# Optimization experiments

Measured on AMD Instinct MI355X. Metric: run time of the kernel, lower is better.

The kernel has to match this reference:

```python
import jax, jax.numpy as jnp
import numpy as np

B, S, D = 4, 2048, 2048          # batch, seq_len, num_hiddens (= query/key/value size)
H = 16                           # num_heads
DH = D // H                      # head dim = shared K/V projection dim


def setup_inputs() -> dict:
    key = jax.random.key(0)
    ks = jax.random.split(key, 11)
    s_in = 1.0 / np.sqrt(D)
    return {
        "q": jax.random.normal(ks[0], (B, S, D), jnp.float32),
        "k": jax.random.normal(ks[1], (B, S, D), jnp.float32),
        "v": jax.random.normal(ks[2], (B, S, D), jnp.float32),
        "Wq": jax.random.normal(ks[3], (D, D), jnp.float32) * s_in,
        "bq": jnp.zeros((D,), jnp.float32),
        "Wk": jax.random.normal(ks[4], (D, DH), jnp.float32) * s_in,
        "bk": jnp.zeros((DH,), jnp.float32),
        "Wv": jax.random.normal(ks[5], (D, DH), jnp.float32) * s_in,
        "bv": jnp.zeros((DH,), jnp.float32),
        "Wo": jax.random.normal(ks[6], (D, D), jnp.float32) * s_in,
        "bo": jnp.zeros((D,), jnp.float32),
    }


def reference(q, k, v, Wq, bq, Wk, bk, Wv, bv, Wo, bo):
    # Projections
    qh = (q @ Wq + bq).reshape(B, S, H, DH).transpose(0, 2, 1, 3)  # [B,H,S,DH]
    kh = k @ Wk + bk                                               # [B,S,DH] shared K head
    vh = v @ Wv + bv                                               # [B,S,DH] shared V head
    # Scaled dot-product attention with broadcast-shared K/V (no copies)
    scores = jnp.einsum('bhqd,bkd->bhqk', qh, kh) / jnp.sqrt(jnp.float32(DH))
    attn = jax.nn.softmax(scores, axis=-1)                          # [B,H,S,S]
    out = jnp.einsum('bhqk,bkd->bhqd', attn, vh)                    # [B,H,S,DH]
    out = out.transpose(0, 2, 1, 3).reshape(B, S, D)                # merge heads
    return out @ Wo + bo
```

## Files before the change

### kernel.cpp

```cpp
#include <hip/hip_runtime.h>
#include <stdint.h>

#define B_  4
#define S_  2048
#define D_  2048
#define H_  16
#define DH_ 128
#define M_  (B_*S_)

typedef unsigned short u16;
typedef __bf16 bf16x8 __attribute__((ext_vector_type(8)));
typedef float  f32x4  __attribute__((ext_vector_type(4)));
typedef u16    u16x4  __attribute__((ext_vector_type(4)));

__device__ __forceinline__ u16 f2bf(float f){
  unsigned x = __float_as_uint(f);
  x += 0x7fffu + ((x >> 16) & 1u);
  return (u16)(x >> 16);
}

__device__ __forceinline__ unsigned pkbf(float lo, float hi){
  unsigned r;
  asm("v_cvt_pk_bf16_f32 %0, %1, %2" : "=v"(r) : "v"(lo), "v"(hi));
  return r;
}

__device__ __forceinline__ void stage16(const void* g, void* lds_base){
  __builtin_amdgcn_global_load_lds(
      (const __attribute__((address_space(1))) void*)g,
      (__attribute__((address_space(3))) void*)lds_base, 16, 0, 0);
}

__device__ __forceinline__ f32x4 mfma16(bf16x8 a, bf16x8 b, f32x4 c){
  return __builtin_amdgcn_mfma_f32_16x16x32_bf16(a, b, c, 0, 0, 0);
}

__global__ void cvt_bf16(const float* __restrict__ s, u16* __restrict__ d, int n4){
  int i = blockIdx.x * 256 + threadIdx.x;
  if (i >= n4) return;
  float4 f = ((const float4*)s)[i];
  u16x4 u = { f2bf(f.x), f2bf(f.y), f2bf(f.z), f2bf(f.w) };
  ((u16x4*)d)[i] = u;
}

__global__ void cvt_bf16_2(const float* __restrict__ s0, const float* __restrict__ s1,
                           u16* __restrict__ d0, u16* __restrict__ d1, int n4){
  const float* s = blockIdx.y ? s1 : s0;
  u16*        d = blockIdx.y ? d1 : d0;
  int i = blockIdx.x * 256 + threadIdx.x;
  if (i >= n4) return;
  float4 f = ((const float4*)s)[i];
  u16x4 u = { f2bf(f.x), f2bf(f.y), f2bf(f.z), f2bf(f.w) };
  ((u16x4*)d)[i] = u;
}

__global__ void transpose_bf(const float* __restrict__ W, u16* __restrict__ WT, int K, int N){
  __shared__ float tl[32][33];
  int n0 = blockIdx.x * 32, k0 = blockIdx.y * 32;
  int tx = threadIdx.x, ty = threadIdx.y;
  for (int r = 0; r < 4; r++)
    tl[ty + 8*r][tx] = W[(size_t)(k0 + ty + 8*r) * N + n0 + tx];
  __syncthreads();
  for (int r = 0; r < 4; r++)
    WT[(size_t)(n0 + ty + 8*r) * K + k0 + tx] = f2bf(tl[tx][ty + 8*r]);
}

__global__ void transpose_vh(const u16* __restrict__ vh, u16* __restrict__ vhT){
  __shared__ u16 tl[32][33];
  int b = blockIdx.z, d0 = blockIdx.x * 32, s0 = blockIdx.y * 32;
  int tx = threadIdx.x, ty = threadIdx.y;
  for (int r = 0; r < 4; r++)
    tl[ty + 8*r][tx] = vh[(size_t)(b * S_ + s0 + ty + 8*r) * DH_ + d0 + tx];
  __syncthreads();
  for (int r = 0; r < 4; r++)
    vhT[(size_t)(b * DH_ + d0 + ty + 8*r) * S_ + s0 + tx] = tl[tx][ty + 8*r];
}

template<int OUTF32>
__global__ __launch_bounds__(512, 1) void gemm256(const u16* __restrict__ A,
    const u16* __restrict__ BT, const float* __restrict__ bias, void* __restrict__ Cv)
{
  __shared__ alignas(16) u16 AB[2][2][2 * 128 * 64];
  const int t = threadIdx.x, lane = t & 63, wave = t >> 6;
  const int quad = lane >> 4, lcol = lane & 15;
  const int wr = wave >> 1, wc = wave & 1;
  const int bid = blockIdx.x;
  const int swz = (bid & 7) * 32 + (bid >> 3);
  const int n0 = (swz & 7) * 256, m0 = (swz >> 3) * 256;
  const int NT = 2048 / 64;

  auto stageH = [&](const u16* g, int grow0, int kcol0, u16* lb){
    #pragma unroll
    for (int i = 0; i < 2; i++){
      int l = (i*8 + wave)*64 + lane;
      int row = l >> 3, st = l & 7;
      int c = st ^ (row & 7);
      stage16(g + (size_t)(grow0 + row)*2048 + kcol0 + c*8, lb + (size_t)(i*8 + wave)*512);
    }
  };

  f32x4 acc[4][2][4] = {};

  stageH(A,  m0,       0,  &AB[0][0][0]);
  stageH(BT, n0,       0,  &AB[0][1][0]);
  stageH(BT, n0 + 128, 0,  &AB[0][1][8192]);
  stageH(A,  m0 + 128, 0,  &AB[0][0][8192]);
  stageH(A,  m0,       64, &AB[1][0][0]);
  stageH(BT, n0 + 128, 64, &AB[1][1][8192]);
  asm volatile("s_waitcnt vmcnt(4)" ::: "memory");
  __builtin_amdgcn_s_barrier();

  for (int T = 0; T < NT; ++T) {
    const int bi = T & 1;
    const u16* Ab = &AB[bi][0][0];
    const u16* Bb = &AB[bi][1][0];
    #pragma unroll
    for (int q = 0; q < 4; ++q) {
      const int ah = q >> 1, bh = (q >> 1) ^ (q & 1);
      bf16x8 af[2][2], bv[4][2];
      #pragma unroll
      for (int m = 0; m < 2; m++) {
        const u16* ap = Ab + (size_t)(ah*128 + wr*32 + m*16 + lcol) * 64;
        #pragma unroll
        for (int kk = 0; kk < 2; kk++)
          af[m][kk] = *(const bf16x8*)(ap + (((kk*4 + quad) ^ (lcol & 7)) * 8));
      }
      #pragma unroll
      for (int n = 0; n < 4; n++) {
        const u16* bp = Bb + (size_t)(bh*128 + wc*64 + n*16 + lcol) * 64;
        #pragma unroll
        for (int kk = 0; kk < 2; kk++)
          bv[n][kk] = *(const bf16x8*)(bp + (((kk*4 + quad) ^ (lcol & 7)) * 8));
      }
      if      (q == 0 && T + 1 < NT) stageH(BT, n0,       (T+1)*64, &AB[(T+1)&1][1][0]);
      else if (q == 1 && T + 1 < NT) stageH(A,  m0 + 128, (T+1)*64, &AB[(T+1)&1][0][8192]);
      else if (q == 2 && T + 2 < NT) stageH(A,  m0,       (T+2)*64, &AB[bi][0][0]);
      else if (q == 3 && T + 2 < NT) stageH(BT, n0 + 128, (T+2)*64, &AB[bi][1][8192]);

      __builtin_amdgcn_s_barrier();
      asm volatile("s_waitcnt lgkmcnt(0)" ::: "memory");
      __builtin_amdgcn_sched_barrier(0);
      __builtin_amdgcn_s_setprio(1);
      #pragma unroll
      for (int m = 0; m < 2; m++)
        #pragma unroll
        for (int n = 0; n < 4; n++)
          #pragma unroll
          for (int kk = 0; kk < 2; kk++)
            acc[q][m][n] = mfma16(af[m][kk], bv[n][kk], acc[q][m][n]);
      __builtin_amdgcn_s_setprio(0);
      if (q == 3) {
        if (T < NT - 2) { asm volatile("s_waitcnt vmcnt(4)" ::: "memory"); }
        else            { asm volatile("s_waitcnt vmcnt(0)" ::: "memory"); }
      }
      __builtin_amdgcn_s_barrier();
    }
  }

  #pragma unroll
  for (int q = 0; q < 4; ++q) {
    const int ah = q >> 1, bh = (q >> 1) ^ (q & 1);
    #pragma unroll
    for (int n = 0; n < 4; n++) {
      int col = n0 + bh*128 + wc*64 + n*16 + lcol;
      float bj = bias[col];
      #pragma unroll
      for (int m = 0; m < 2; m++) {
        int rowb = m0 + ah*128 + wr*32 + m*16 + quad*4;
        #pragma unroll
        for (int r = 0; r < 4; r++) {
          float vv = acc[q][m][n][r] + bj;
          if (OUTF32) ((float*)Cv)[(size_t)(rowb + r) * 2048 + col] = vv;
          else        ((u16*)Cv)  [(size_t)(rowb + r) * 2048 + col] = f2bf(vv);
        }
      }
    }
  }
}

__global__ __launch_bounds__(256) void gemm_kv(
    const u16* __restrict__ A0, const u16* __restrict__ A1,
    const u16* __restrict__ BT0, const u16* __restrict__ BT1,
    const float* __restrict__ b0, const float* __restrict__ b1,
    u16* __restrict__ C0, u16* __restrict__ C1)
{
  const int sel = blockIdx.z;
  const u16* A  = sel ? A1 : A0;
  const u16* BT = sel ? BT1 : BT0;
  const float* bias = sel ? b1 : b0;
  u16* C = sel ? C1 : C0;

  __shared__ alignas(16) u16 Al[32 * 32];
  __shared__ alignas(16) u16 Bl[128 * 32];
  const int t = threadIdx.x, lane = t & 63, wave = t >> 6;
  const int quad = lane >> 4, lcol = lane & 15;
  const int m0 = blockIdx.x * 32;

  f32x4 acc[2][2] = {};
  for (int k0 = 0; k0 < D_; k0 += 32) {
    if (t < 128) {
      int row = t >> 2, kc = t & 3;
      stage16(A + (size_t)(m0 + row) * D_ + k0 + kc * 8, Al + (wave * 64) * 8);
    } else {
      int bc = t - 128, row = bc >> 2, kc = bc & 3;
      stage16(BT + (size_t)row * D_ + k0 + kc * 8, Bl + ((wave - 2) * 64) * 8);
    }
    {
      int bc = t + 128, row = bc >> 2, kc = bc & 3;
      stage16(BT + (size_t)row * D_ + k0 + kc * 8, Bl + (128 + wave * 64) * 8);
    }
    if (t < 128) {
      int bc = t + 384, row = bc >> 2, kc = bc & 3;
      stage16(BT + (size_t)row * D_ + k0 + kc * 8, Bl + (384 + wave * 64) * 8);
    }
    __syncthreads();
    bf16x8 af[2], bfr[2];
    for (int i = 0; i < 2; i++)
      af[i]  = *(const bf16x8*)(Al + (i*16 + lcol) * 32 + quad * 8);
    for (int j = 0; j < 2; j++)
      bfr[j] = *(const bf16x8*)(Bl + (wave*32 + j*16 + lcol) * 32 + quad * 8);
    for (int i = 0; i < 2; i++)
      for (int j = 0; j < 2; j++)
        acc[i][j] = mfma16(af[i], bfr[j], acc[i][j]);
    __syncthreads();
  }
  for (int j = 0; j < 2; j++) {
    int n = wave * 32 + j * 16 + lcol;
    float bj = bias[n];
    for (int i = 0; i < 2; i++) {
      int mbase = m0 + i * 16 + quad * 4;
      for (int r = 0; r < 4; r++)
        C[(size_t)(mbase + r) * DH_ + n] = f2bf(acc[i][j][r] + bj);
    }
  }
}

__global__ __launch_bounds__(256, 3) void mqa_attn(const u16* __restrict__ qh,
    const u16* __restrict__ kh, const u16* __restrict__ vhT, u16* __restrict__ ao)
{
  __shared__ alignas(16) u16 Kl[2][32 * 128];
  __shared__ alignas(16) u16 Vl[2][128 * 32];
  const int t = threadIdx.x, lane = t & 63, wave = t >> 6;
  const int quad = lane >> 4, lcol = lane & 15;
  const int b = blockIdx.z, h = blockIdx.y;
  const int q0 = blockIdx.x * 128 + wave * 32;
  const float sc2 = 0.12751743f;

  bf16x8 qf[2][4];
  for (int m = 0; m < 2; m++) {
    const u16* qp = qh + (size_t)(b * S_ + q0 + m * 16 + lcol) * D_ + h * DH_ + quad * 8;
    for (int kk = 0; kk < 4; kk++) qf[m][kk] = *(const bf16x8*)(qp + kk * 32);
  }
  union { u16 u[8]; bf16x8 v; } one_u;
  for (int i = 0; i < 8; i++) one_u.u[i] = 0x3F80;
  const bf16x8 ones = one_u.v;

  f32x4 o[2][8] = {};
  f32x4 al[2] = {};
  const u16* kb = kh  + (size_t)b * S_ * DH_;
  const u16* vb = vhT + (size_t)b * DH_ * S_;

  auto stageKV = [&](int tt, int bi) {
    int kv0 = tt * 32;
    for (int p = 0; p < 2; p++) {
      int c = p * 256 + wave * 64 + lane;
      int row = c >> 4, st = c & 15;
      int kc = st ^ (row & 15);
      stage16(kb + (size_t)(kv0 + row) * DH_ + kc * 8, &Kl[bi][(p*256 + wave*64) * 8]);
    }
    for (int p = 0; p < 2; p++) {
      int c = p * 256 + wave * 64 + lane;
      int row = c >> 2, st = c & 3;
      int kc = st ^ (row & 3) ^ ((row >> 2) & 3);
      stage16(vb + (size_t)row * S_ + kv0 + kc * 8, &Vl[bi][(p*256 + wave*64) * 8]);
    }
  };

  stageKV(0, 0);
  for (int tt = 0; tt < S_ / 32; tt++) {
    const int bi = tt & 1;
    __syncthreads();
    if (tt < S_ / 32 - 1) stageKV(tt + 1, bi ^ 1);

    const u16* Kb = &Kl[bi][0];
    const u16* Vb = &Vl[bi][0];

    unsigned cc[2][4];
    for (int kvf = 0; kvf < 2; kvf++) {
      f32x4 s[2] = {};
      const u16* kp = Kb + (size_t)(kvf * 16 + lcol) * 128;
      __builtin_amdgcn_s_setprio(1);
      for (int kk = 0; kk < 4; kk++) {
        int swz = (kk * 4 + quad) ^ lcol;
        bf16x8 kfr = *(const bf16x8*)(kp + swz * 8);
        for (int m = 0; m < 2; m++)
          s[m] = mfma16(kfr, qf[m][kk], s[m]);
      }
      __builtin_amdgcn_s_setprio(0);
      for (int m = 0; m < 2; m++) {
        float e0 = exp2f(s[m][0] * sc2), e1 = exp2f(s[m][1] * sc2);
        float e2 = exp2f(s[m][2] * sc2), e3 = exp2f(s[m][3] * sc2);
        cc[m][kvf * 2 + 0] = pkbf(e0, e1);
        cc[m][kvf * 2 + 1] = pkbf(e2, e3);
      }
    }
    bf16x8 pa[2];
    for (int m = 0; m < 2; m++) {
      asm("v_permlane32_swap_b32 %0, %1" : "+v"(cc[m][0]), "+v"(cc[m][2]));
      asm("v_permlane16_swap_b32 %0, %1" : "+v"(cc[m][0]), "+v"(cc[m][2]));
      asm("v_permlane32_swap_b32 %0, %1" : "+v"(cc[m][1]), "+v"(cc[m][3]));
      asm("v_permlane16_swap_b32 %0, %1" : "+v"(cc[m][1]), "+v"(cc[m][3]));
      union { unsigned u[4]; bf16x8 v; } pu;
      pu.u[0] = cc[m][0];
      pu.u[1] = cc[m][1];
      pu.u[2] = cc[m][2];
      pu.u[3] = cc[m][3];
      pa[m] = pu.v;
    }

    __builtin_amdgcn_s_setprio(1);
    for (int g = 0; g < 8; g++) {
      int swz = quad ^ (lcol & 3) ^ ((lcol >> 2) & 3);
      bf16x8 vfr = *(const bf16x8*)(Vb + (size_t)(g * 16 + lcol) * 32 + swz * 8);
      for (int m = 0; m < 2; m++)
        o[m][g] = mfma16(pa[m], vfr, o[m][g]);
    }
    for (int m = 0; m < 2; m++)
      al[m] = mfma16(pa[m], ones, al[m]);
    __builtin_amdgcn_s_setprio(0);
  }

  for (int m = 0; m < 2; m++) {
    u16* op = ao + (size_t)(b * S_ + q0 + m * 16 + quad * 4) * D_ + h * DH_ + lcol;
    for (int r = 0; r < 4; r++) {
      float inv = 1.0f / al[m][r];
      for (int g = 0; g < 8; g++)
        op[(size_t)r * D_ + g * 16] = f2bf(o[m][g][r] * inv);
    }
  }
}

extern "C" void kernel_launch(void* const* d_in, const int* in_sizes, int n_in,
                              void* d_out, int out_size, void* d_ws, size_t ws_size,
                              hipStream_t stream)
{
  (void)in_sizes; (void)n_in; (void)out_size;
  const float* q  = (const float*)d_in[0];
  const float* k  = (const float*)d_in[1];
  const float* v  = (const float*)d_in[2];
  const float* Wq = (const float*)d_in[3];
  const float* bq = (const float*)d_in[4];
  const float* Wk = (const float*)d_in[5];
  const float* bk = (const float*)d_in[6];
  const float* Wv = (const float*)d_in[7];
  const float* bv = (const float*)d_in[8];
  const float* Wo = (const float*)d_in[9];
  const float* bo = (const float*)d_in[10];
  float* out = (float*)d_out;

  char* ws = (char*)d_ws;
  size_t off = 0;
  auto alloc = [&](size_t bytes) -> char* {
    char* p = ws + off; off += (bytes + 255) & ~(size_t)255; return p;
  };
  u16* xbf = (u16*)alloc((size_t)M_ * D_ * 2);
  u16* qh  = (u16*)alloc((size_t)M_ * D_ * 2);
  u16* kh  = (u16*)alloc((size_t)M_ * DH_ * 2);
  u16* vh  = (u16*)alloc((size_t)M_ * DH_ * 2);
  u16* vhT = (u16*)alloc((size_t)M_ * DH_ * 2);
  u16* WqT = (u16*)alloc((size_t)D_ * D_ * 2);
  u16* WkT = (u16*)alloc((size_t)DH_ * D_ * 2);
  u16* WvT = (u16*)alloc((size_t)DH_ * D_ * 2);
  u16* WoT = (u16*)alloc((size_t)D_ * D_ * 2);
  u16* ao  = xbf;

  if (off > ws_size) return;

  const int n4 = M_ * D_ / 4;

  transpose_bf<<<dim3(D_/32,  D_/32), dim3(32, 8), 0, stream>>>(Wq, WqT, D_, D_);
  transpose_bf<<<dim3(DH_/32, D_/32), dim3(32, 8), 0, stream>>>(Wk, WkT, D_, DH_);
  transpose_bf<<<dim3(DH_/32, D_/32), dim3(32, 8), 0, stream>>>(Wv, WvT, D_, DH_);
  transpose_bf<<<dim3(D_/32,  D_/32), dim3(32, 8), 0, stream>>>(Wo, WoT, D_, D_);

  cvt_bf16_2<<<dim3(n4 / 256, 2), dim3(256), 0, stream>>>(k, v, xbf, qh, n4);
  gemm_kv<<<dim3(M_/32, 1, 2), dim3(256), 0, stream>>>(
      xbf, qh, WkT, WvT, bk, bv, kh, vh);
  transpose_vh<<<dim3(DH_/32, S_/32, B_), dim3(32, 8), 0, stream>>>(vh, vhT);
  cvt_bf16<<<dim3(n4 / 256), dim3(256), 0, stream>>>(q, xbf, n4);
  gemm256<0><<<dim3(256), dim3(512), 0, stream>>>(xbf, WqT, bq, qh);

  mqa_attn<<<dim3(S_/128, H_, B_), dim3(256), 0, stream>>>(qh, kh, vhT, ao);

  gemm256<1><<<dim3(256), dim3(512), 0, stream>>>(ao, WoT, bo, out);
}
```

Measured before the change: 600.6 us.

## Switch gemm256 to 32x32x16 MFMA and restructure into two half-tile phases

```diff
diff --git a/kernel.cpp b/kernel.cpp
--- a/kernel.cpp
+++ b/kernel.cpp
@@ -11,6 +11,7 @@
 typedef unsigned short u16;
 typedef __bf16 bf16x8 __attribute__((ext_vector_type(8)));
 typedef float  f32x4  __attribute__((ext_vector_type(4)));
+typedef float  f32x16 __attribute__((ext_vector_type(16)));
 typedef u16    u16x4  __attribute__((ext_vector_type(4)));
 
 __device__ __forceinline__ u16 f2bf(float f){
@@ -33,6 +34,9 @@
 
 __device__ __forceinline__ f32x4 mfma16(bf16x8 a, bf16x8 b, f32x4 c){
   return __builtin_amdgcn_mfma_f32_16x16x32_bf16(a, b, c, 0, 0, 0);
+}
+__device__ __forceinline__ f32x16 mfma32(bf16x8 a, bf16x8 b, f32x16 c){
+  return __builtin_amdgcn_mfma_f32_32x32x16_bf16(a, b, c, 0, 0, 0);
 }
 
 __global__ void cvt_bf16(const float* __restrict__ s, u16* __restrict__ d, int n4){
@@ -82,7 +86,7 @@
 {
   __shared__ alignas(16) u16 AB[2][2][2 * 128 * 64];
   const int t = threadIdx.x, lane = t & 63, wave = t >> 6;
-  const int quad = lane >> 4, lcol = lane & 15;
+  const int hi = lane >> 5, l31 = lane & 31, l7 = lane & 7;
   const int wr = wave >> 1, wc = wave & 1;
   const int bid = blockIdx.x;
   const int swz = (bid & 7) * 32 + (bid >> 3);
@@ -99,7 +103,7 @@
     }
   };
 
-  f32x4 acc[4][2][4] = {};
+  f32x16 acc[2][2][2] = {};
 
   stageH(A,  m0,       0,  &AB[0][0][0]);
   stageH(BT, n0,       0,  &AB[0][1][0]);
@@ -114,68 +118,86 @@
     const int bi = T & 1;
     const u16* Ab = &AB[bi][0][0];
     const u16* Bb = &AB[bi][1][0];
-    #pragma unroll
-    for (int q = 0; q < 4; ++q) {
-      const int ah = q >> 1, bh = (q >> 1) ^ (q & 1);
-      bf16x8 af[2][2], bv[4][2];
-      #pragma unroll
-      for (int m = 0; m < 2; m++) {
-        const u16* ap = Ab + (size_t)(ah*128 + wr*32 + m*16 + lcol) * 64;
+    bf16x8 af[2][4];
+    bf16x8 bv[2][4];
+
+    #pragma unroll
+    for (int ah = 0; ah < 2; ah++) {
+      const u16* ap = Ab + (size_t)(ah*128 + wr*32 + l31) * 64;
+      #pragma unroll
+      for (int ks = 0; ks < 4; ks++)
+        af[ah][ks] = *(const bf16x8*)(ap + (((ks*2 + hi) ^ l7) * 8));
+    }
+    #pragma unroll
+    for (int nf = 0; nf < 2; nf++) {
+      const u16* bp = Bb + (size_t)(wc*64 + nf*32 + l31) * 64;
+      #pragma unroll
+      for (int ks = 0; ks < 4; ks++)
+        bv[nf][ks] = *(const bf16x8*)(bp + (((ks*2 + hi) ^ l7) * 8));
+    }
+    if (T + 1 < NT) {
+      stageH(BT, n0,       (T+1)*64, &AB[(T+1)&1][1][0]);
+      stageH(A,  m0 + 128, (T+1)*64, &AB[(T+1)&1][0][8192]);
+    }
+    __builtin_amdgcn_s_barrier();
+    asm volatile("s_waitcnt lgkmcnt(0)" ::: "memory");
+    __builtin_amdgcn_sched_barrier(0);
+    __builtin_amdgcn_s_setprio(1);
+    #pragma unroll
+    for (int ah = 0; ah < 2; ah++)
+      #pragma unroll
+      for (int nf = 0; nf < 2; nf++)
         #pragma unroll
-        for (int kk = 0; kk < 2; kk++)
-          af[m][kk] = *(const bf16x8*)(ap + (((kk*4 + quad) ^ (lcol & 7)) * 8));
-      }
-      #pragma unroll
-      for (int n = 0; n < 4; n++) {
-        const u16* bp = Bb + (size_t)(bh*128 + wc*64 + n*16 + lcol) * 64;
+        for (int ks = 0; ks < 4; ks++)
+          acc[ah][0][nf] = mfma32(af[ah][ks], bv[nf][ks], acc[ah][0][nf]);
+    __builtin_amdgcn_s_setprio(0);
+    __builtin_amdgcn_s_barrier();
+
+    if (T + 2 < NT)
+      stageH(A,  m0,       (T+2)*64, &AB[bi][0][0]);
+    #pragma unroll
+    for (int nf = 0; nf < 2; nf++) {
+      const u16* bp = Bb + (size_t)(128 + wc*64 + nf*32 + l31) * 64;
+      #pragma unroll
+      for (int ks = 0; ks < 4; ks++)
+        bv[nf][ks] = *(const bf16x8*)(bp + (((ks*2 + hi) ^ l7) * 8));
+    }
+    __builtin_amdgcn_s_barrier();
+    asm volatile("s_waitcnt lgkmcnt(0)" ::: "memory");
+    __builtin_amdgcn_sched_barrier(0);
+    if (T + 2 < NT)
+      stageH(BT, n0 + 128, (T+2)*64, &AB[bi][1][8192]);
+    __builtin_amdgcn_s_setprio(1);
+    #pragma unroll
+    for (int ah = 0; ah < 2; ah++)
+      #pragma unroll
+      for (int nf = 0; nf < 2; nf++)
         #pragma unroll
-        for (int kk = 0; kk < 2; kk++)
-          bv[n][kk] = *(const bf16x8*)(bp + (((kk*4 + quad) ^ (lcol & 7)) * 8));
-      }
-      if      (q == 0 && T + 1 < NT) stageH(BT, n0,       (T+1)*64, &AB[(T+1)&1][1][0]);
-      else if (q == 1 && T + 1 < NT) stageH(A,  m0 + 128, (T+1)*64, &AB[(T+1)&1][0][8192]);
-      else if (q == 2 && T + 2 < NT) stageH(A,  m0,       (T+2)*64, &AB[bi][0][0]);
-      else if (q == 3 && T + 2 < NT) stageH(BT, n0 + 128, (T+2)*64, &AB[bi][1][8192]);
-
-      __builtin_amdgcn_s_barrier();
-      asm volatile("s_waitcnt lgkmcnt(0)" ::: "memory");
-      __builtin_amdgcn_sched_barrier(0);
-      __builtin_amdgcn_s_setprio(1);
-      #pragma unroll
-      for (int m = 0; m < 2; m++)
+        for (int ks = 0; ks < 4; ks++)
+          acc[ah][1][nf] = mfma32(af[ah][ks], bv[nf][ks], acc[ah][1][nf]);
+    __builtin_amdgcn_s_setprio(0);
+    if (T < NT - 2) { asm volatile("s_waitcnt vmcnt(4)" ::: "memory"); }
+    else            { asm volatile("s_waitcnt vmcnt(0)" ::: "memory"); }
+    __builtin_amdgcn_s_barrier();
+  }
+
+  #pragma unroll
+  for (int ah = 0; ah < 2; ah++)
+    #pragma unroll
+    for (int bh = 0; bh < 2; bh++)
+      #pragma unroll
+      for (int nf = 0; nf < 2; nf++) {
+        int col = n0 + bh*128 + wc*64 + nf*32 + l31;
+        float bj = bias[col];
+        int rowb = m0 + ah*128 + wr*32 + 4*hi;
         #pragma unroll
-        for (int n = 0; n < 4; n++)
-          #pragma unroll
-          for (int kk = 0; kk < 2; kk++)
-            acc[q][m][n] = mfma16(af[m][kk], bv[n][kk], acc[q][m][n]);
-      __builtin_amdgcn_s_setprio(0);
-      if (q == 3) {
-        if (T < NT - 2) { asm volatile("s_waitcnt vmcnt(4)" ::: "memory"); }
-        else            { asm volatile("s_waitcnt vmcnt(0)" ::: "memory"); }
-      }
-      __builtin_amdgcn_s_barrier();
-    }
-  }
-
-  #pragma unroll
-  for (int q = 0; q < 4; ++q) {
-    const int ah = q >> 1, bh = (q >> 1) ^ (q & 1);
-    #pragma unroll
-    for (int n = 0; n < 4; n++) {
-      int col = n0 + bh*128 + wc*64 + n*16 + lcol;
-      float bj = bias[col];
-      #pragma unroll
-      for (int m = 0; m < 2; m++) {
-        int rowb = m0 + ah*128 + wr*32 + m*16 + quad*4;
-        #pragma unroll
-        for (int r = 0; r < 4; r++) {
-          float vv = acc[q][m][n][r] + bj;
-          if (OUTF32) ((float*)Cv)[(size_t)(rowb + r) * 2048 + col] = vv;
-          else        ((u16*)Cv)  [(size_t)(rowb + r) * 2048 + col] = f2bf(vv);
+        for (int rg = 0; rg < 16; rg++) {
+          int row = rowb + (rg & 3) + 8*(rg >> 2);
+          float vv = acc[ah][bh][nf][rg] + bj;
+          if (OUTF32) ((float*)Cv)[(size_t)row * 2048 + col] = vv;
+          else        ((u16*)Cv)  [(size_t)row * 2048 + col] = f2bf(vv);
         }
       }
-    }
-  }
 }
 
 __global__ __launch_bounds__(256) void gemm_kv(
```

Result: no change. 598.2 us (-0.4%).
